# Kernel tuning notes

Hardware: AMD Instinct MI355X
Metric: run time of the kernel (lower is better)

## Reference

```python
import jax, jax.numpy as jnp
import numpy as np

D = 128
H = 4
DK = D // H


def _spmm(row, col, val, x, n):
    # sparse.mm(adj, x) with adj in COO form: out[row] += val * x[col]
    return jax.ops.segment_sum(val[:, None] * x[col], row, num_segments=n)


def _arrg(h, a1_w, a1_b, a2_w, a2_b):
    return jax.nn.leaky_relu(h @ a1_w + a1_b, negative_slope=0.01) @ a2_w + a2_b


def _cross_attn(x, q_x, q_w, k_w, v_w):
    n, d = x.shape
    m = q_x.shape[0]
    q = (q_x @ q_w).reshape(m, H, DK).transpose(1, 0, 2)   # [H, Q, dk]
    k = (x @ k_w).reshape(n, H, DK).transpose(1, 0, 2)     # [H, N, dk]
    v = (q_x @ v_w).reshape(m, H, DK).transpose(1, 0, 2)   # [H, Q, dk]
    s = jnp.einsum('hnd,hqd->hnq', k, q) / jnp.sqrt(jnp.float32(DK))
    w = jax.nn.softmax(s, axis=-1)                          # softmax over queries
    out = jnp.einsum('hnq,hqd->hnd', w, v).transpose(1, 0, 2).reshape(n, d)
    return out + x


def setup_inputs() -> dict:
    key = jax.random.key(0)
    ks = iter(jax.random.split(key, 64))
    nrm = lambda shape, s=0.05: jax.random.normal(next(ks), shape, jnp.float32) * s
    inp = {}
    inp['trans_w'] = nrm((1, D)); inp['trans_b'] = nrm((D,))
    inp['g_w'] = nrm((D, D));     inp['g_b'] = nrm((D,))
    inp['qg_w'] = nrm((D, D));    inp['qg_b'] = nrm((D,))
    inp['q_w'] = nrm((D, D)); inp['k_w'] = nrm((D, D)); inp['v_w'] = nrm((D, D))
    inp['a1_w'] = nrm((D, 2 * D)); inp['a1_b'] = nrm((2 * D,))
    inp['a2_w'] = nrm((2 * D, D)); inp['a2_b'] = nrm((D,))
    inp['x0'] = jax.random.normal(next(ks), (25000,), jnp.float32)
    inp['q0'] = jax.random.normal(next(ks), (100,), jnp.float32)
    for i in (1, 2, 3):
        inp[f'xin{i}'] = jax.random.normal(next(ks), (25000,), jnp.float32)
        inp[f'qin{i}'] = jax.random.normal(next(ks), (100,), jnp.float32)
    n_sizes = {1: 50000, 2: 75000, 3: 100000}
    q_sizes = {1: 200, 2: 300, 3: 400}
    for i in (1, 2, 3):
        e = 16 * n_sizes[i]
        inp[f'aval{i}'] = jax.random.uniform(next(ks), (e,), jnp.float32)
        inp[f'arow{i}'] = jax.random.randint(next(ks), (e,), 0, n_sizes[i], jnp.int64)
        inp[f'acol{i}'] = jax.random.randint(next(ks), (e,), 0, n_sizes[i], jnp.int64)
        qe = 16 * q_sizes[i]
        inp[f'qval{i}'] = jax.random.uniform(next(ks), (qe,), jnp.float32)
        inp[f'qrow{i}'] = jax.random.randint(next(ks), (qe,), 0, q_sizes[i], jnp.int64)
        inp[f'qcol{i}'] = jax.random.randint(next(ks), (qe,), 0, q_sizes[i], jnp.int64)
    return inp


def reference(trans_w, trans_b, g_w, g_b, qg_w, qg_b, q_w, k_w, v_w,
              a1_w, a1_b, a2_w, a2_b,
              x0, q0, xin1, xin2, xin3, qin1, qin2, qin3,
              aval1, aval2, aval3, qval1, qval2, qval3,
              arow1, acol1, arow2, acol2, arow3, acol3,
              qrow1, qcol1, qrow2, qcol2, qrow3, qcol3):
    trans = lambda v: v[:, None] @ trans_w + trans_b
    x = trans(x0)
    qx = trans(q0)
    steps = [
        (xin1, qin1, arow1, acol1, aval1, qrow1, qcol1, qval1, 50000, 200),
        (xin2, qin2, arow2, acol2, aval2, qrow2, qcol2, qval2, 75000, 300),
        (xin3, qin3, arow3, acol3, aval3, qrow3, qcol3, qval3, 100000, 400),
    ]
    for xin, qin, ar, ac, av, qr, qc, qv, n, m in steps:
        x = jnp.concatenate([x, trans(xin)], axis=0)
        qx = jnp.concatenate([qx, trans(qin)], axis=0)
        x = _spmm(ar, ac, av, x @ g_w + g_b, n)
        qx = _spmm(qr, qc, qv, qx @ qg_w + qg_b, m)
        x = _arrg(x, a1_w, a1_b, a2_w, a2_b)
        qx = _arrg(qx, a1_w, a1_b, a2_w, a2_b)
        x = _cross_attn(x, qx, q_w, k_w, v_w)
    return (x, qx)
```

## Files before the change

kernel.cpp:

```cpp
#include <hip/hip_runtime.h>

typedef unsigned short u16;
typedef __attribute__((ext_vector_type(8))) short bf16x8;
typedef __attribute__((ext_vector_type(4))) float f32x4;

__device__ __forceinline__ float b2f(u16 v) {
    return __uint_as_float(((unsigned)v) << 16);
}
__device__ __forceinline__ u16 f2b(float x) {
    unsigned u = __float_as_uint(x);
    unsigned r = u + 0x7FFFu + ((u >> 16) & 1u);
    return (u16)(r >> 16);
}
__device__ __forceinline__ float4 load_bf4(const u16* p) {
    ushort4 q = *(const ushort4*)p;
    float4 f;
    f.x = b2f(q.x); f.y = b2f(q.y); f.z = b2f(q.z); f.w = b2f(q.w);
    return f;
}
__device__ __forceinline__ float4 in4(const void* p, long off, bool bf) {
    if (bf) return load_bf4((const u16*)p + off);
    return *(const float4*)((const float*)p + off);
}
__device__ __forceinline__ float in1(const void* p, long off, bool bf) {
    if (bf) return b2f(((const u16*)p)[off]);
    return ((const float*)p)[off];
}
__device__ __forceinline__ int inIdx(const void* p, long i, bool i64) {
    return ((const int*)p)[i64 ? 2 * i : i];
}

__global__ void sniff_kernel(const u16* __restrict__ x0bits, const int* __restrict__ arow,
                             int* __restrict__ flags) {
    if (threadIdx.x != 0 || blockIdx.x != 0) return;
    int plaus = 0;
    for (int i = 0; i < 256; ++i) {
        u16 v = x0bits[i];
        int e = (v >> 7) & 0xFF;
        if (v == 0 || (e >= 100 && e <= 135)) plaus++;
    }
    flags[0] = (plaus >= 200) ? 1 : 0;
    int nz = 0;
    for (int i = 1; i < 128; i += 2) nz += (arow[i] != 0);
    flags[1] = (nz == 0) ? 1 : 0;
}

__global__ void trans_kernel(const void* __restrict__ v, const void* __restrict__ tw,
                             const void* __restrict__ tb, float* __restrict__ out,
                             int rows, const int* __restrict__ flags) {
    const bool bf = flags[0] != 0;
    int t = blockIdx.x * blockDim.x + threadIdx.x;
    int c4 = (t & 31) * 4;
    int r = t >> 5;
    if (r >= rows) return;
    float vv = in1(v, r, bf);
    float4 w4 = in4(tw, c4, bf);
    float4 b4 = in4(tb, c4, bf);
    float4 o;
    o.x = vv * w4.x + b4.x; o.y = vv * w4.y + b4.y;
    o.z = vv * w4.z + b4.z; o.w = vv * w4.w + b4.w;
    *(float4*)(out + (size_t)r * 128 + c4) = o;
}

__global__ void wprep_kernel(const void* __restrict__ src, u16* __restrict__ dst,
                             int K, int N, const int* __restrict__ flags) {
    const bool bf = flags[0] != 0;
    int idx = blockIdx.x * blockDim.x + threadIdx.x;
    if (idx >= K * N) return;
    int j = idx & 7, lane = (idx >> 3) & 63, t = idx >> 9;
    int KC = K >> 5;
    int kc = t % KC, ct = t / KC;
    int k = kc * 32 + (lane >> 4) * 8 + j;
    int nn = ct * 16 + (lane & 15);
    dst[idx] = f2b(in1(src, (long)k * N + nn, bf));
}

template<int KTOT, int NOUT, bool LEAKY, typename AT, typename CT>
__launch_bounds__(256)
__global__ void gemm_mfma_kernel(const AT* __restrict__ A, const u16* __restrict__ Wf,
                                 const void* __restrict__ bias, CT* __restrict__ C,
                                 int n, const int* __restrict__ flags) {
    constexpr int KC = KTOT / 32;
    constexpr int NT = NOUT / 16;
    __shared__ u16 wlds[KTOT * NOUT];
    {
        const int4* srcw = (const int4*)Wf;
        int4* dstw = (int4*)wlds;
        constexpr int NV = KTOT * NOUT * 2 / 16;
#pragma unroll
        for (int i = 0; i < NV / 256; ++i)
            dstw[i * 256 + threadIdx.x] = srcw[i * 256 + threadIdx.x];
    }
    __syncthreads();
    const bool bf = flags[0] != 0;
    const int lane = threadIdx.x & 63;
    const int wave = threadIdx.x >> 6;
    const int quad = lane >> 4, col = lane & 15;
    const int rbase = (blockIdx.x * 4 + wave) * 16;
    if (rbase >= n) return;
    int node = rbase + col; if (node >= n) node = n - 1;
    f32x4 acc[NT];
#pragma unroll
    for (int ct = 0; ct < NT; ++ct) acc[ct] = (f32x4){0.f, 0.f, 0.f, 0.f};
#pragma unroll
    for (int kc = 0; kc < KC; ++kc) {
        bf16x8 af;
        if constexpr (sizeof(AT) == 2) {
            af = *(const bf16x8*)((const u16*)A + (size_t)node * KTOT + kc * 32 + quad * 8);
        } else {
            const float* ap = (const float*)A + (size_t)node * KTOT + kc * 32 + quad * 8;
            float4 a0 = *(const float4*)ap;
            float4 a1 = *(const float4*)(ap + 4);
            af[0] = (short)f2b(a0.x); af[1] = (short)f2b(a0.y);
            af[2] = (short)f2b(a0.z); af[3] = (short)f2b(a0.w);
            af[4] = (short)f2b(a1.x); af[5] = (short)f2b(a1.y);
            af[6] = (short)f2b(a1.z); af[7] = (short)f2b(a1.w);
        }
#pragma unroll
        for (int ct = 0; ct < NT; ++ct) {
            bf16x8 wf = *(const bf16x8*)(wlds + (((ct * KC + kc) * 64 + lane) * 8));
            acc[ct] = __builtin_amdgcn_mfma_f32_16x16x32_bf16(af, wf, acc[ct], 0, 0, 0);
        }
    }
#pragma unroll
    for (int ct = 0; ct < NT; ++ct) {
        int colg = ct * 16 + col;
        float b = bias ? in1(bias, colg, bf) : 0.f;
#pragma unroll
        for (int r = 0; r < 4; ++r) {
            int row = rbase + quad * 4 + r;
            if (row >= n) continue;
            float v = acc[ct][r] + b;
            if (LEAKY) v = v > 0.f ? v : 0.01f * v;
            if constexpr (sizeof(CT) == 2) C[(size_t)row * NOUT + colg] = (CT)f2b(v);
            else                           C[(size_t)row * NOUT + colg] = (CT)v;
        }
    }
}

#define RSH 8
#define NBC_MAX 512
#define EPB 4096

__global__ void zero_int_kernel(int* __restrict__ p, int n) {
    int i = blockIdx.x * blockDim.x + threadIdx.x;
    if (i < n) p[i] = 0;
}

__global__ void bhist_kernel(const void* __restrict__ rows, int e, int* __restrict__ bcnt,
                             int nbc, const int* __restrict__ flags) {
    __shared__ int hist[NBC_MAX];
    const bool i64 = flags[1] != 0;
    for (int i = threadIdx.x; i < nbc; i += 256) hist[i] = 0;
    __syncthreads();
    int base = blockIdx.x * 8192;
    int end = base + 8192; if (end > e) end = e;
    for (int i = base + threadIdx.x; i < end; i += 256)
        atomicAdd(&hist[inIdx(rows, i, i64) >> RSH], 1);
    __syncthreads();
    for (int i = threadIdx.x; i < nbc; i += 256) {
        int c = hist[i];
        if (c) atomicAdd(&bcnt[i], c);
    }
}

__global__ void scanA_kernel(const int* __restrict__ cnt, int n, int* __restrict__ bsum) {
    int base = blockIdx.x * 2048;
    int s = 0;
    for (int j = threadIdx.x; j < 2048; j += 256) {
        int idx = base + j;
        if (idx < n) s += cnt[idx];
    }
#pragma unroll
    for (int off = 32; off; off >>= 1) s += __shfl_down(s, off);
    __shared__ int ws[4];
    if ((threadIdx.x & 63) == 0) ws[threadIdx.x >> 6] = s;
    __syncthreads();
    if (threadIdx.x == 0) bsum[blockIdx.x] = ws[0] + ws[1] + ws[2] + ws[3];
}
__global__ void scanB_kernel(int* __restrict__ bsum, int nb) {
    if (threadIdx.x == 0) {
        int acc = 0;
        for (int i = 0; i < nb; ++i) { int v = bsum[i]; bsum[i] = acc; acc += v; }
    }
}
__global__ void scanC_kernel(const int* __restrict__ cnt, int n, const int* __restrict__ bsum,
                             int* __restrict__ optr, int* __restrict__ ocur) {
    __shared__ int tsum[256];
    int base = blockIdx.x * 2048 + threadIdx.x * 8;
    int v[8]; int s = 0;
#pragma unroll
    for (int j = 0; j < 8; ++j) {
        int idx = base + j;
        v[j] = (idx < n) ? cnt[idx] : 0;
        s += v[j];
    }
    tsum[threadIdx.x] = s;
    __syncthreads();
    for (int off = 1; off < 256; off <<= 1) {
        int t = (threadIdx.x >= off) ? tsum[threadIdx.x - off] : 0;
        __syncthreads();
        tsum[threadIdx.x] += t;
        __syncthreads();
    }
    int excl = bsum[blockIdx.x] + tsum[threadIdx.x] - s;
#pragma unroll
    for (int j = 0; j < 8; ++j) {
        int idx = base + j;
        if (idx < n) { optr[idx] = excl; ocur[idx] = excl; }
        excl += v[j];
    }
}

__launch_bounds__(256)
__global__ void psort_kernel(const void* __restrict__ rows, const void* __restrict__ colsin,
                             const void* __restrict__ valsin, int e,
                             int* __restrict__ gcur, int2* __restrict__ pack0,
                             int nbc, const int* __restrict__ flags) {
    __shared__ int hist[NBC_MAX];
    __shared__ int scan[NBC_MAX];
    __shared__ int base[NBC_MAX];
    __shared__ int cur[NBC_MAX];
    __shared__ int2 stage[EPB];
    __shared__ u16 binof[EPB];
    const bool bf = flags[0] != 0;
    const bool i64 = flags[1] != 0;
    const int tid = threadIdx.x;
    const long s0 = (long)blockIdx.x * EPB;
    int cnt_e = e - (int)s0; if (cnt_e > EPB) cnt_e = EPB;

    for (int i = tid; i < NBC_MAX; i += 256) hist[i] = 0;
    __syncthreads();
    for (int j = tid; j < cnt_e; j += 256)
        atomicAdd(&hist[inIdx(rows, s0 + j, i64) >> RSH], 1);
    __syncthreads();
    for (int i = tid; i < NBC_MAX; i += 256) scan[i] = hist[i];
    __syncthreads();
    for (int off = 1; off < NBC_MAX; off <<= 1) {
        int a = (tid >= off) ? scan[tid - off] : 0;
        int c = scan[tid + 256 - off];
        __syncthreads();
        scan[tid] += a;
        scan[tid + 256] += c;
        __syncthreads();
    }
    for (int i = tid; i < nbc; i += 256) {
        int h = hist[i];
        cur[i] = scan[i] - h;
        base[i] = h ? atomicAdd(&gcur[i], h) : 0;
    }
    __syncthreads();
    for (int j = tid; j < cnt_e; j += 256) {
        int r = inIdx(rows, s0 + j, i64);
        int bin = r >> RSH;
        int p = atomicAdd(&cur[bin], 1);
        int2 pk;
        pk.x = ((r & ((1 << RSH) - 1)) << 20) | inIdx(colsin, s0 + j, i64);
        pk.y = __float_as_int(in1(valsin, s0 + j, bf));
        stage[p] = pk;
        binof[p] = (u16)bin;
    }
    __syncthreads();
    for (int j = tid; j < cnt_e; j += 256) {
        int bin = binof[j];
        int st = scan[bin] - hist[bin];
        pack0[base[bin] + (j - st)] = stage[j];
    }
}

__launch_bounds__(256)
__global__ void breorder256_kernel(const int2* __restrict__ pack0, const int* __restrict__ bptr,
                                   const int* __restrict__ bend, int2* __restrict__ pack1,
                                   int* __restrict__ rowptr, int* __restrict__ rowend, int n) {
    __shared__ int hist[256], scan[256], cur[256];
    const int b = blockIdx.x;
    const int s = bptr[b], e = bend[b];
    const int tid = threadIdx.x;
    hist[tid] = 0;
    __syncthreads();
    for (int i = s + tid; i < e; i += 256)
        atomicAdd(&hist[(unsigned)pack0[i].x >> 20], 1);
    __syncthreads();
    scan[tid] = hist[tid];
    __syncthreads();
    for (int off = 1; off < 256; off <<= 1) {
        int a = (tid >= off) ? scan[tid - off] : 0;
        __syncthreads();
        scan[tid] += a;
        __syncthreads();
    }
    int st = s + scan[tid] - hist[tid];
    cur[tid] = st;
    int rg = (b << RSH) + tid;
    if (rg < n) { rowptr[rg] = st; rowend[rg] = st + hist[tid]; }
    __syncthreads();
    for (int i = s + tid; i < e; i += 256) {
        int2 pk = pack0[i];
        int rl = (unsigned)pk.x >> 20;
        int p = atomicAdd(&cur[rl], 1);
        pack1[p] = (int2){pk.x & 0xFFFFF, pk.y};
    }
}

__device__ __forceinline__ f32x4 bffma4(float v, uint2 h, f32x4 a) {
    a[0] += v * __uint_as_float(h.x << 16);
    a[1] += v * __uint_as_float(h.x & 0xFFFF0000u);
    a[2] += v * __uint_as_float(h.y << 16);
    a[3] += v * __uint_as_float(h.y & 0xFFFF0000u);
    return a;
}
__global__ void spmm_kernel(const u16* __restrict__ H, const int* __restrict__ rowptr,
                            const int* __restrict__ rowend, const int2* __restrict__ pack,
                            u16* __restrict__ out, int n) {
    int w = threadIdx.x >> 6;
    int lane = threadIdx.x & 63;
    int r = blockIdx.x * 4 + w;
    if (r >= n) return;
    const int half = lane >> 5;
    const int l5 = lane & 31;
    int s = rowptr[r], e = rowend[r];
    f32x4 acc = {0.f, 0.f, 0.f, 0.f};
    int i = s + half;
    for (; i + 6 < e; i += 8) {
        int2 p0 = pack[i], p1 = pack[i + 2], p2 = pack[i + 4], p3 = pack[i + 6];
        uint2 h0 = *(const uint2*)(H + (size_t)p0.x * 128 + l5 * 4);
        uint2 h1 = *(const uint2*)(H + (size_t)p1.x * 128 + l5 * 4);
        uint2 h2 = *(const uint2*)(H + (size_t)p2.x * 128 + l5 * 4);
        uint2 h3 = *(const uint2*)(H + (size_t)p3.x * 128 + l5 * 4);
        acc = bffma4(__int_as_float(p0.y), h0, acc);
        acc = bffma4(__int_as_float(p1.y), h1, acc);
        acc = bffma4(__int_as_float(p2.y), h2, acc);
        acc = bffma4(__int_as_float(p3.y), h3, acc);
    }
    for (; i < e; i += 2) {
        int2 p0 = pack[i];
        uint2 h0 = *(const uint2*)(H + (size_t)p0.x * 128 + l5 * 4);
        acc = bffma4(__int_as_float(p0.y), h0, acc);
    }
    acc[0] += __shfl_xor(acc[0], 32, 64);
    acc[1] += __shfl_xor(acc[1], 32, 64);
    acc[2] += __shfl_xor(acc[2], 32, 64);
    acc[3] += __shfl_xor(acc[3], 32, 64);
    if (half == 0) {
        ushort4 o;
        o.x = f2b(acc[0]); o.y = f2b(acc[1]); o.z = f2b(acc[2]); o.w = f2b(acc[3]);
        *(ushort4*)(out + (size_t)r * 128 + l5 * 4) = o;
    }
}

__global__ void attn_prep_kernel(const float* __restrict__ Qq, const float* __restrict__ Qv,
                                 u16* __restrict__ Qf, u16* __restrict__ Vf,
                                 int m, int mt32) {
    int idx = blockIdx.x * blockDim.x + threadIdx.x;
    int total = 4 * mt32 * 1024;
    if (idx >= total) return;
    const int mt16 = mt32 * 2;
    const float scale = 0.17677669529663687f;
    {
        int j = idx & 7, lane = (idx >> 3) & 63;
        int t = idx >> 9;
        int h = t / mt16, qt = t - h * mt16;
        int dim = ((lane >> 4) & 3) * 8 + j;
        int query = qt * 16 + (lane & 15);
        Qf[idx] = (query < m) ? f2b(Qq[(size_t)query * 128 + h * 32 + dim] * scale) : (u16)0;
    }
    {
        int j = idx & 7, lane = (idx >> 3) & 63;
        int u = idx >> 9;
        int dh = u & 1, t = u >> 1;
        int h = t / mt32, qc = t - h * mt32;
        int query = qc * 32 + ((lane >> 4) & 3) * 8 + j;
        int dim = dh * 16 + (lane & 15);
        Vf[idx] = (query < m) ? f2b(Qv[(size_t)query * 128 + h * 32 + dim]) : (u16)0;
    }
}

__launch_bounds__(256)
__global__ void attn_mfma_kernel(const u16* __restrict__ Kb, const u16* __restrict__ Qf,
                                 const u16* __restrict__ Vf, float* __restrict__ X,
                                 int n, int m, int mt32, int pad) {
    __shared__ u16 Pbuf_all[4 * 16 * 40];
    const int h = blockIdx.y;
    const int wave = threadIdx.x >> 6;
    const int lane = threadIdx.x & 63;
    u16* Pbuf = Pbuf_all + wave * 16 * 40;
    const int nb = (blockIdx.x * 4 + wave) * 16;
    if (nb >= n) return;
    const int quad = lane >> 4, col = lane & 15;
    int node = nb + col; if (node >= n) node = n - 1;
    bf16x8 kf = *(const bf16x8*)(Kb + (size_t)node * 128 + h * 32 + quad * 8);
    f32x4 O0 = {0.f, 0.f, 0.f, 0.f}, O1 = {0.f, 0.f, 0.f, 0.f};
    const f32x4 zero = {0.f, 0.f, 0.f, 0.f};
    float Lp0 = 0.f, Lp1 = 0.f, Lp2 = 0.f, Lp3 = 0.f;
    const u16* Qbase = Qf + (size_t)h * (mt32 * 2) * 512;
    const u16* Vbase = Vf + (size_t)h * mt32 * 1024;
    for (int qc = 0; qc < mt32; ++qc) {
#pragma unroll
        for (int half = 0; half < 2; ++half) {
            bf16x8 qfr = *(const bf16x8*)(Qbase + (size_t)(qc * 2 + half) * 512 + lane * 8);
            f32x4 S = __builtin_amdgcn_mfma_f32_16x16x32_bf16(kf, qfr, zero, 0, 0, 0);
            float e0 = __expf(fminf(S[0], 80.f));
            float e1 = __expf(fminf(S[1], 80.f));
            float e2 = __expf(fminf(S[2], 80.f));
            float e3 = __expf(fminf(S[3], 80.f));
            Lp0 += e0; Lp1 += e1; Lp2 += e2; Lp3 += e3;
            int qoff = half * 16 + col;
            Pbuf[(quad * 4 + 0) * 40 + qoff] = f2b(e0);
            Pbuf[(quad * 4 + 1) * 40 + qoff] = f2b(e1);
            Pbuf[(quad * 4 + 2) * 40 + qoff] = f2b(e2);
            Pbuf[(quad * 4 + 3) * 40 + qoff] = f2b(e3);
        }
        bf16x8 pf = *(const bf16x8*)(Pbuf + col * 40 + quad * 8);
        bf16x8 v0 = *(const bf16x8*)(Vbase + (size_t)(qc * 2 + 0) * 512 + lane * 8);
        bf16x8 v1 = *(const bf16x8*)(Vbase + (size_t)(qc * 2 + 1) * 512 + lane * 8);
        O0 = __builtin_amdgcn_mfma_f32_16x16x32_bf16(pf, v0, O0, 0, 0, 0);
        O1 = __builtin_amdgcn_mfma_f32_16x16x32_bf16(pf, v1, O1, 0, 0, 0);
    }
#pragma unroll
    for (int mask = 1; mask < 16; mask <<= 1) {
        Lp0 += __shfl_xor(Lp0, mask, 64);
        Lp1 += __shfl_xor(Lp1, mask, 64);
        Lp2 += __shfl_xor(Lp2, mask, 64);
        Lp3 += __shfl_xor(Lp3, mask, 64);
    }
    float inv[4];
    inv[0] = 1.f / fmaxf(Lp0 - (float)pad, 1e-35f);
    inv[1] = 1.f / fmaxf(Lp1 - (float)pad, 1e-35f);
    inv[2] = 1.f / fmaxf(Lp2 - (float)pad, 1e-35f);
    inv[3] = 1.f / fmaxf(Lp3 - (float)pad, 1e-35f);
#pragma unroll
    for (int r = 0; r < 4; ++r) {
        int nd = nb + quad * 4 + r;
        if (nd < n) {
            float* xp = X + (size_t)nd * 128 + h * 32;
            xp[col]      += O0[r] * inv[r];
            xp[16 + col] += O1[r] * inv[r];
        }
    }
}

__global__ void out_writer_kernel(const float* __restrict__ in, void* __restrict__ out,
                                  long elem_off, int n4, const int* __restrict__ flags) {
    const bool bf = flags[0] != 0;
    int i = blockIdx.x * blockDim.x + threadIdx.x;
    if (i >= n4) return;
    float4 v = ((const float4*)in)[i];
    if (bf) {
        ushort4 q; q.x = f2b(v.x); q.y = f2b(v.y); q.z = f2b(v.z); q.w = f2b(v.w);
        ((ushort4*)((u16*)out + elem_off))[i] = q;
    } else {
        ((float4*)((float*)out + elem_off))[i] = v;
    }
}

extern "C" void kernel_launch(void* const* d_in, const int* in_sizes, int n_in,
                              void* d_out, int out_size, void* d_ws, size_t ws_size,
                              hipStream_t stream) {
    (void)n_in; (void)out_size; (void)ws_size;
    const void* trans_w = d_in[0];
    const void* trans_b = d_in[1];
    const void* g_w  = d_in[2];
    const void* g_b  = d_in[3];
    const void* qg_w = d_in[4];
    const void* qg_b = d_in[5];
    const void* q_w  = d_in[6];
    const void* k_w  = d_in[7];
    const void* v_w  = d_in[8];
    const void* a1_w = d_in[9];
    const void* a1_b = d_in[10];
    const void* a2_w = d_in[11];
    const void* a2_b = d_in[12];
    const void* x0   = d_in[13];
    const void* q0   = d_in[14];

    int ixin[3], iqin[3], iaval[3], iarow[3], iacol[3], iqval[3], iqrow[3], iqcol[3];
    if (in_sizes[16] == 100) {
        for (int s = 0; s < 3; ++s) {
            ixin[s] = 15 + 2 * s; iqin[s] = 16 + 2 * s;
            int b = 21 + 6 * s;
            iaval[s] = b; iarow[s] = b + 1; iacol[s] = b + 2;
            iqval[s] = b + 3; iqrow[s] = b + 4; iqcol[s] = b + 5;
        }
    } else {
        int xs[3] = {15,16,17}, qs_[3] = {18,19,20};
        int av[3] = {21,22,23}, qv[3] = {24,25,26};
        int ar[3] = {27,29,31}, ac[3] = {28,30,32};
        int qr[3] = {33,35,37}, qc[3] = {34,36,38};
        for (int s = 0; s < 3; ++s) {
            ixin[s]=xs[s]; iqin[s]=qs_[s]; iaval[s]=av[s]; iqval[s]=qv[s];
            iarow[s]=ar[s]; iacol[s]=ac[s]; iqrow[s]=qr[s]; iqcol[s]=qc[s];
        }
    }

    char* p = (char*)d_ws;
    auto alloc = [&](size_t bytes) -> char* {
        char* r = p;
        p += (bytes + 255) & ~(size_t)255;
        return r;
    };
    int*   flags = (int*)alloc(256);
    const int NMAX = 100000;
    float* X   = (float*)alloc((size_t)NMAX * 128 * 4);
    u16*   T1b = (u16*)  alloc((size_t)NMAX * 128 * 2);
    u16*   Xs  = (u16*)  alloc((size_t)NMAX * 128 * 2);
    u16*   T2  = (u16*)  alloc((size_t)NMAX * 256 * 2);
    float* QX  = (float*)alloc((size_t)400 * 128 * 4);
    u16*   QT1b= (u16*)  alloc((size_t)400 * 128 * 2);
    u16*   QXs = (u16*)  alloc((size_t)400 * 128 * 2);
    u16*   QT2 = (u16*)  alloc((size_t)400 * 256 * 2);
    float* Qq  = (float*)alloc((size_t)400 * 128 * 4);
    float* Qv  = (float*)alloc((size_t)400 * 128 * 4);
    u16*   Qfrag = (u16*)alloc((size_t)4 * 13 * 1024 * 2);
    u16*   Vfrag = (u16*)alloc((size_t)4 * 13 * 1024 * 2);
    u16* Wg  = (u16*)alloc((size_t)128 * 128 * 2);
    u16* Wqg = (u16*)alloc((size_t)128 * 128 * 2);
    u16* Wa1 = (u16*)alloc((size_t)128 * 256 * 2);
    u16* Wa2 = (u16*)alloc((size_t)256 * 128 * 2);
    u16* Wk  = (u16*)alloc((size_t)128 * 128 * 2);
    u16* Wq  = (u16*)alloc((size_t)128 * 128 * 2);
    u16* Wv  = (u16*)alloc((size_t)128 * 128 * 2);
    int2*  csr_pack = (int2*)alloc((size_t)1600000 * 8);
    int*   bcnt   = (int*)alloc((size_t)NBC_MAX * 4);
    int*   bktptr = (int*)alloc((size_t)NBC_MAX * 4);
    int*   bktcur = (int*)alloc((size_t)NBC_MAX * 4);
    int*   rowptr = (int*)alloc((size_t)NMAX * 4);
    int*   rowend = (int*)alloc((size_t)NMAX * 4);
    int*   bsum   = (int*)alloc(256);
    int2*  pack0  = (int2*)T2;

    sniff_kernel<<<1, 64, 0, stream>>>((const u16*)x0, (const int*)d_in[iarow[0]], flags);

    auto wprep = [&](const void* src, u16* dst, int K, int N) {
        wprep_kernel<<<(K * N + 255) / 256, 256, 0, stream>>>(src, dst, K, N, flags);
    };
    wprep(g_w,  Wg,  128, 128);
    wprep(qg_w, Wqg, 128, 128);
    wprep(a1_w, Wa1, 128, 256);
    wprep(a2_w, Wa2, 256, 128);
    wprep(k_w,  Wk,  128, 128);
    wprep(q_w,  Wq,  128, 128);
    wprep(v_w,  Wv,  128, 128);

    auto launch_trans = [&](const void* v, float* out, int rows) {
        trans_kernel<<<(rows * 32 + 255) / 256, 256, 0, stream>>>(v, trans_w, trans_b, out, rows, flags);
    };
    auto build_spmm = [&](const void* rows, const void* colsidx, const void* vals, int e,
                          int nrows, const u16* H, u16* OUT) {
        int nbc = (nrows + 255) >> RSH;
        int nsb = (nbc + 2047) / 2048;
        zero_int_kernel<<<(nbc + 255) / 256, 256, 0, stream>>>(bcnt, nbc);
        bhist_kernel<<<(e + 8191) / 8192, 256, 0, stream>>>(rows, e, bcnt, nbc, flags);
        scanA_kernel<<<nsb, 256, 0, stream>>>(bcnt, nbc, bsum);
        scanB_kernel<<<1, 64, 0, stream>>>(bsum, nsb);
        scanC_kernel<<<nsb, 256, 0, stream>>>(bcnt, nbc, bsum, bktptr, bktcur);
        psort_kernel<<<(e + EPB - 1) / EPB, 256, 0, stream>>>(rows, colsidx, vals, e,
                                                              bktcur, pack0, nbc, flags);
        breorder256_kernel<<<nbc, 256, 0, stream>>>(pack0, bktptr, bktcur, csr_pack,
                                                    rowptr, rowend, nrows);
        spmm_kernel<<<(nrows + 3) / 4, 256, 0, stream>>>(H, rowptr, rowend, csr_pack,
                                                         OUT, nrows);
    };

    int nprev = in_sizes[13];
    int mprev = in_sizes[14];
    launch_trans(x0, X, nprev);
    launch_trans(q0, QX, mprev);

    const int ns[3] = {50000, 75000, 100000};
    const int ms[3] = {200, 300, 400};
    for (int s = 0; s < 3; ++s) {
        const int n = ns[s], m = ms[s];
        const int e  = in_sizes[iaval[s]];
        const int qe = in_sizes[iqval[s]];
        launch_trans(d_in[ixin[s]], X + (size_t)nprev * 128, n - nprev);
        launch_trans(d_in[iqin[s]], QX + (size_t)mprev * 128, m - mprev);
        const int gb  = (n + 63) / 64;
        const int gqb = (m + 63) / 64;
        gemm_mfma_kernel<128, 128, false, float, u16><<<gb, 256, 0, stream>>>(X, Wg, g_b, T1b, n, flags);
        build_spmm(d_in[iarow[s]], d_in[iacol[s]], d_in[iaval[s]], e, n, T1b, Xs);
        gemm_mfma_kernel<128, 128, false, float, u16><<<gqb, 256, 0, stream>>>(QX, Wqg, qg_b, QT1b, m, flags);
        build_spmm(d_in[iqrow[s]], d_in[iqcol[s]], d_in[iqval[s]], qe, m, QT1b, QXs);
        gemm_mfma_kernel<128, 256, true, u16, u16><<<gb, 256, 0, stream>>>(Xs, Wa1, a1_b, T2, n, flags);
        gemm_mfma_kernel<256, 128, false, u16, float><<<gb, 256, 0, stream>>>(T2, Wa2, a2_b, X, n, flags);
        gemm_mfma_kernel<128, 256, true, u16, u16><<<gqb, 256, 0, stream>>>(QXs, Wa1, a1_b, QT2, m, flags);
        gemm_mfma_kernel<256, 128, false, u16, float><<<gqb, 256, 0, stream>>>(QT2, Wa2, a2_b, QX, m, flags);
        gemm_mfma_kernel<128, 128, false, float, u16><<<gb, 256, 0, stream>>>(X, Wk, nullptr, T1b, n, flags);
        gemm_mfma_kernel<128, 128, false, float, float><<<gqb, 256, 0, stream>>>(QX, Wq, nullptr, Qq, m, flags);
        gemm_mfma_kernel<128, 128, false, float, float><<<gqb, 256, 0, stream>>>(QX, Wv, nullptr, Qv, m, flags);
        const int mt32 = (m + 31) / 32;
        const int pad = mt32 * 32 - m;
        const int ptot = 4 * mt32 * 1024;
        attn_prep_kernel<<<(ptot + 255) / 256, 256, 0, stream>>>(Qq, Qv, Qfrag, Vfrag, m, mt32);
        attn_mfma_kernel<<<dim3((n + 63) / 64, 4), 256, 0, stream>>>(T1b, Qfrag, Vfrag, X, n, m, mt32, pad);
        nprev = n;
        mprev = m;
    }

    const int n4x = 100000 * 128 / 4;
    const int n4q = 400 * 128 / 4;
    out_writer_kernel<<<(n4x + 255) / 256, 256, 0, stream>>>(X, d_out, 0, n4x, flags);
    out_writer_kernel<<<(n4q + 255) / 256, 256, 0, stream>>>(QX, d_out, (long)100000 * 128, n4q, flags);
}
```

Measured before the change: 1.327 ms.

## Widen attention tiles, use exp2 and transpose-read LDS, fuse Q/V GEMMs and scans

The attention kernel now handles 32 nodes per wave instead of 16, so each Q and V fragment load is shared by two K tiles. It folds log2(e) into the Q scale so it can use the native exp2, packs probabilities with v_cvt_pk_bf16_f32, and reads them back with ds_read_b64_tr_b16 transpose loads. Separately, the Q and V projections are fused into one kernel that shares the A-tile load, and the three-kernel bucket scan is replaced by a single-block scan. This removes several small launches and redundant loads, at the cost of more registers per wave and hand-written inline asm with manual waitcnts.

```diff
diff --git a/kernel.cpp b/kernel.cpp
--- a/kernel.cpp
+++ b/kernel.cpp
@@ -3,6 +3,7 @@
 typedef unsigned short u16;
 typedef __attribute__((ext_vector_type(8))) short bf16x8;
 typedef __attribute__((ext_vector_type(4))) float f32x4;
+typedef __attribute__((ext_vector_type(2))) unsigned u32x2;
 
 __device__ __forceinline__ float b2f(u16 v) {
     return __uint_as_float(((unsigned)v) << 16);
@@ -138,6 +139,67 @@
     }
 }
 
+__launch_bounds__(256)
+__global__ void gemm_qv_kernel(const float* __restrict__ A, const u16* __restrict__ Wfq,
+                               const u16* __restrict__ Wfv, float* __restrict__ Cq,
+                               float* __restrict__ Cv, int n) {
+    __shared__ u16 wldsq[128 * 128];
+    __shared__ u16 wldsv[128 * 128];
+    {
+        const int4* sq = (const int4*)Wfq;
+        const int4* sv = (const int4*)Wfv;
+        int4* dq = (int4*)wldsq;
+        int4* dv = (int4*)wldsv;
+#pragma unroll
+        for (int i = 0; i < 8; ++i) {
+            dq[i * 256 + threadIdx.x] = sq[i * 256 + threadIdx.x];
+            dv[i * 256 + threadIdx.x] = sv[i * 256 + threadIdx.x];
+        }
+    }
+    __syncthreads();
+    const int lane = threadIdx.x & 63;
+    const int wave = threadIdx.x >> 6;
+    const int quad = lane >> 4, col = lane & 15;
+    const int rbase = (blockIdx.x * 4 + wave) * 16;
+    if (rbase >= n) return;
+    int node = rbase + col; if (node >= n) node = n - 1;
+    f32x4 accq[8], accv[8];
+#pragma unroll
+    for (int ct = 0; ct < 8; ++ct) {
+        accq[ct] = (f32x4){0.f, 0.f, 0.f, 0.f};
+        accv[ct] = (f32x4){0.f, 0.f, 0.f, 0.f};
+    }
+#pragma unroll
+    for (int kc = 0; kc < 4; ++kc) {
+        const float* ap = A + (size_t)node * 128 + kc * 32 + quad * 8;
+        float4 a0 = *(const float4*)ap;
+        float4 a1 = *(const float4*)(ap + 4);
+        bf16x8 af;
+        af[0] = (short)f2b(a0.x); af[1] = (short)f2b(a0.y);
+        af[2] = (short)f2b(a0.z); af[3] = (short)f2b(a0.w);
+        af[4] = (short)f2b(a1.x); af[5] = (short)f2b(a1.y);
+        af[6] = (short)f2b(a1.z); af[7] = (short)f2b(a1.w);
+#pragma unroll
+        for (int ct = 0; ct < 8; ++ct) {
+            bf16x8 wq = *(const bf16x8*)(wldsq + (((ct * 4 + kc) * 64 + lane) * 8));
+            bf16x8 wv = *(const bf16x8*)(wldsv + (((ct * 4 + kc) * 64 + lane) * 8));
+            accq[ct] = __builtin_amdgcn_mfma_f32_16x16x32_bf16(af, wq, accq[ct], 0, 0, 0);
+            accv[ct] = __builtin_amdgcn_mfma_f32_16x16x32_bf16(af, wv, accv[ct], 0, 0, 0);
+        }
+    }
+#pragma unroll
+    for (int ct = 0; ct < 8; ++ct) {
+        int colg = ct * 16 + col;
+#pragma unroll
+        for (int r = 0; r < 4; ++r) {
+            int row = rbase + quad * 4 + r;
+            if (row >= n) continue;
+            Cq[(size_t)row * 128 + colg] = accq[ct][r];
+            Cv[(size_t)row * 128 + colg] = accv[ct][r];
+        }
+    }
+}
+
 #define RSH 8
 #define NBC_MAX 512
 #define EPB 4096
@@ -164,52 +226,24 @@
     }
 }
 
-__global__ void scanA_kernel(const int* __restrict__ cnt, int n, int* __restrict__ bsum) {
-    int base = blockIdx.x * 2048;
-    int s = 0;
-    for (int j = threadIdx.x; j < 2048; j += 256) {
-        int idx = base + j;
-        if (idx < n) s += cnt[idx];
-    }
-#pragma unroll
-    for (int off = 32; off; off >>= 1) s += __shfl_down(s, off);
-    __shared__ int ws[4];
-    if ((threadIdx.x & 63) == 0) ws[threadIdx.x >> 6] = s;
-    __syncthreads();
-    if (threadIdx.x == 0) bsum[blockIdx.x] = ws[0] + ws[1] + ws[2] + ws[3];
-}
-__global__ void scanB_kernel(int* __restrict__ bsum, int nb) {
-    if (threadIdx.x == 0) {
-        int acc = 0;
-        for (int i = 0; i < nb; ++i) { int v = bsum[i]; bsum[i] = acc; acc += v; }
-    }
-}
-__global__ void scanC_kernel(const int* __restrict__ cnt, int n, const int* __restrict__ bsum,
+__global__ void scanF_kernel(const int* __restrict__ bcnt, int nbc,
                              int* __restrict__ optr, int* __restrict__ ocur) {
-    __shared__ int tsum[256];
-    int base = blockIdx.x * 2048 + threadIdx.x * 8;
-    int v[8]; int s = 0;
-#pragma unroll
-    for (int j = 0; j < 8; ++j) {
-        int idx = base + j;
-        v[j] = (idx < n) ? cnt[idx] : 0;
-        s += v[j];
-    }
-    tsum[threadIdx.x] = s;
-    __syncthreads();
-    for (int off = 1; off < 256; off <<= 1) {
-        int t = (threadIdx.x >= off) ? tsum[threadIdx.x - off] : 0;
+    __shared__ int sc[NBC_MAX];
+    const int tid = threadIdx.x;
+    int v0 = (tid < nbc) ? bcnt[tid] : 0;
+    int v1 = (tid + 256 < nbc) ? bcnt[tid + 256] : 0;
+    sc[tid] = v0; sc[tid + 256] = v1;
+    __syncthreads();
+    for (int off = 1; off < NBC_MAX; off <<= 1) {
+        int a = (tid >= off) ? sc[tid - off] : 0;
+        int b = sc[tid + 256 - off];
         __syncthreads();
-        tsum[threadIdx.x] += t;
+        sc[tid] += a;
+        sc[tid + 256] += b;
         __syncthreads();
     }
-    int excl = bsum[blockIdx.x] + tsum[threadIdx.x] - s;
-#pragma unroll
-    for (int j = 0; j < 8; ++j) {
-        int idx = base + j;
-        if (idx < n) { optr[idx] = excl; ocur[idx] = excl; }
-        excl += v[j];
-    }
+    if (tid < nbc)       { int x = sc[tid] - v0;       optr[tid] = x;       ocur[tid] = x; }
+    if (tid + 256 < nbc) { int x = sc[tid + 256] - v1; optr[tid + 256] = x; ocur[tid + 256] = x; }
 }
 
 __launch_bounds__(256)
@@ -355,7 +389,7 @@
     int total = 4 * mt32 * 1024;
     if (idx >= total) return;
     const int mt16 = mt32 * 2;
-    const float scale = 0.17677669529663687f;
+    const float scale = 0.17677669529663687f * 1.44269504088896340736f;
     {
         int j = idx & 7, lane = (idx >> 3) & 63;
         int t = idx >> 9;
@@ -379,62 +413,100 @@
 __global__ void attn_mfma_kernel(const u16* __restrict__ Kb, const u16* __restrict__ Qf,
                                  const u16* __restrict__ Vf, float* __restrict__ X,
                                  int n, int m, int mt32, int pad) {
-    __shared__ u16 Pbuf_all[4 * 16 * 40];
+    __shared__ __align__(128) u16 Pbuf_all[4 * 1024];
     const int h = blockIdx.y;
     const int wave = threadIdx.x >> 6;
     const int lane = threadIdx.x & 63;
-    u16* Pbuf = Pbuf_all + wave * 16 * 40;
-    const int nb = (blockIdx.x * 4 + wave) * 16;
+    const int nb = (blockIdx.x * 4 + wave) * 32;
     if (nb >= n) return;
     const int quad = lane >> 4, col = lane & 15;
-    int node = nb + col; if (node >= n) node = n - 1;
-    bf16x8 kf = *(const bf16x8*)(Kb + (size_t)node * 128 + h * 32 + quad * 8);
-    f32x4 O0 = {0.f, 0.f, 0.f, 0.f}, O1 = {0.f, 0.f, 0.f, 0.f};
+    int node0 = nb + col;      if (node0 >= n) node0 = n - 1;
+    int node1 = nb + 16 + col; if (node1 >= n) node1 = n - 1;
+    bf16x8 kf0 = *(const bf16x8*)(Kb + (size_t)node0 * 128 + h * 32 + quad * 8);
+    bf16x8 kf1 = *(const bf16x8*)(Kb + (size_t)node1 * 128 + h * 32 + quad * 8);
+    f32x4 O00 = {0.f, 0.f, 0.f, 0.f}, O01 = {0.f, 0.f, 0.f, 0.f};
+    f32x4 O10 = {0.f, 0.f, 0.f, 0.f}, O11 = {0.f, 0.f, 0.f, 0.f};
     const f32x4 zero = {0.f, 0.f, 0.f, 0.f};
-    float Lp0 = 0.f, Lp1 = 0.f, Lp2 = 0.f, Lp3 = 0.f;
+    float Lp0[4] = {0.f, 0.f, 0.f, 0.f};
+    float Lp1[4] = {0.f, 0.f, 0.f, 0.f};
+    u16* Pw0 = Pbuf_all + wave * 1024;
+    u16* Pw1 = Pw0 + 512;
+    uint2* pw0[2]; uint2* pw1[2];
+    pw0[0] = (uint2*)(Pw0 + col * 16 + quad * 4);
+    pw0[1] = (uint2*)(Pw0 + 256 + col * 16 + quad * 4);
+    pw1[0] = (uint2*)(Pw1 + col * 16 + quad * 4);
+    pw1[1] = (uint2*)(Pw1 + 256 + col * 16 + quad * 4);
+    const unsigned paddr0 = (unsigned)(uintptr_t)Pw0 + (unsigned)(quad * 256 + col * 8);
+    const unsigned paddr1 = (unsigned)(uintptr_t)Pw1 + (unsigned)(quad * 256 + col * 8);
     const u16* Qbase = Qf + (size_t)h * (mt32 * 2) * 512;
     const u16* Vbase = Vf + (size_t)h * mt32 * 1024;
     for (int qc = 0; qc < mt32; ++qc) {
 #pragma unroll
         for (int half = 0; half < 2; ++half) {
             bf16x8 qfr = *(const bf16x8*)(Qbase + (size_t)(qc * 2 + half) * 512 + lane * 8);
-            f32x4 S = __builtin_amdgcn_mfma_f32_16x16x32_bf16(kf, qfr, zero, 0, 0, 0);
-            float e0 = __expf(fminf(S[0], 80.f));
-            float e1 = __expf(fminf(S[1], 80.f));
-            float e2 = __expf(fminf(S[2], 80.f));
-            float e3 = __expf(fminf(S[3], 80.f));
-            Lp0 += e0; Lp1 += e1; Lp2 += e2; Lp3 += e3;
-            int qoff = half * 16 + col;
-            Pbuf[(quad * 4 + 0) * 40 + qoff] = f2b(e0);
-            Pbuf[(quad * 4 + 1) * 40 + qoff] = f2b(e1);
-            Pbuf[(quad * 4 + 2) * 40 + qoff] = f2b(e2);
-            Pbuf[(quad * 4 + 3) * 40 + qoff] = f2b(e3);
-        }
-        bf16x8 pf = *(const bf16x8*)(Pbuf + col * 40 + quad * 8);
+            f32x4 S0 = __builtin_amdgcn_mfma_f32_16x16x32_bf16(kf0, qfr, zero, 0, 0, 0);
+            f32x4 S1 = __builtin_amdgcn_mfma_f32_16x16x32_bf16(kf1, qfr, zero, 0, 0, 0);
+            float a0 = __builtin_amdgcn_exp2f(fminf(S0[0], 115.f));
+            float a1 = __builtin_amdgcn_exp2f(fminf(S0[1], 115.f));
+            float a2 = __builtin_amdgcn_exp2f(fminf(S0[2], 115.f));
+            float a3 = __builtin_amdgcn_exp2f(fminf(S0[3], 115.f));
+            float b0 = __builtin_amdgcn_exp2f(fminf(S1[0], 115.f));
+            float b1 = __builtin_amdgcn_exp2f(fminf(S1[1], 115.f));
+            float b2 = __builtin_amdgcn_exp2f(fminf(S1[2], 115.f));
+            float b3 = __builtin_amdgcn_exp2f(fminf(S1[3], 115.f));
+            Lp0[0] += a0; Lp0[1] += a1; Lp0[2] += a2; Lp0[3] += a3;
+            Lp1[0] += b0; Lp1[1] += b1; Lp1[2] += b2; Lp1[3] += b3;
+            unsigned ra, rb, rc, rd;
+            asm volatile("v_cvt_pk_bf16_f32 %0, %1, %2" : "=v"(ra) : "v"(a0), "v"(a1));
+            asm volatile("v_cvt_pk_bf16_f32 %0, %1, %2" : "=v"(rb) : "v"(a2), "v"(a3));
+            asm volatile("v_cvt_pk_bf16_f32 %0, %1, %2" : "=v"(rc) : "v"(b0), "v"(b1));
+            asm volatile("v_cvt_pk_bf16_f32 %0, %1, %2" : "=v"(rd) : "v"(b2), "v"(b3));
+            uint2 pka; pka.x = ra; pka.y = rb;
+            uint2 pkb; pkb.x = rc; pkb.y = rd;
+            *pw0[half] = pka;
+            *pw1[half] = pkb;
+        }
+        asm volatile("s_waitcnt lgkmcnt(0)" ::: "memory");
+        u32x2 t0a, t0b, t1a, t1b;
+        asm volatile("ds_read_b64_tr_b16 %0, %1" : "=&v"(t0a) : "v"(paddr0) : "memory");
+        asm volatile("ds_read_b64_tr_b16 %0, %1 offset:128" : "=&v"(t0b) : "v"(paddr0) : "memory");
+        asm volatile("ds_read_b64_tr_b16 %0, %1" : "=&v"(t1a) : "v"(paddr1) : "memory");
+        asm volatile("ds_read_b64_tr_b16 %0, %1 offset:128" : "=&v"(t1b) : "v"(paddr1) : "memory");
+        asm volatile("s_waitcnt lgkmcnt(0)" ::: "memory");
+        __builtin_amdgcn_sched_barrier(0);
+        bf16x8 pf0, pf1;
+        ((u32x2*)&pf0)[0] = t0a; ((u32x2*)&pf0)[1] = t0b;
+        ((u32x2*)&pf1)[0] = t1a; ((u32x2*)&pf1)[1] = t1b;
         bf16x8 v0 = *(const bf16x8*)(Vbase + (size_t)(qc * 2 + 0) * 512 + lane * 8);
         bf16x8 v1 = *(const bf16x8*)(Vbase + (size_t)(qc * 2 + 1) * 512 + lane * 8);
-        O0 = __builtin_amdgcn_mfma_f32_16x16x32_bf16(pf, v0, O0, 0, 0, 0);
-        O1 = __builtin_amdgcn_mfma_f32_16x16x32_bf16(pf, v1, O1, 0, 0, 0);
+        O00 = __builtin_amdgcn_mfma_f32_16x16x32_bf16(pf0, v0, O00, 0, 0, 0);
+        O01 = __builtin_amdgcn_mfma_f32_16x16x32_bf16(pf0, v1, O01, 0, 0, 0);
+        O10 = __builtin_amdgcn_mfma_f32_16x16x32_bf16(pf1, v0, O10, 0, 0, 0);
+        O11 = __builtin_amdgcn_mfma_f32_16x16x32_bf16(pf1, v1, O11, 0, 0, 0);
     }
 #pragma unroll
     for (int mask = 1; mask < 16; mask <<= 1) {
-        Lp0 += __shfl_xor(Lp0, mask, 64);
-        Lp1 += __shfl_xor(Lp1, mask, 64);
-        Lp2 += __shfl_xor(Lp2, mask, 64);
-        Lp3 += __shfl_xor(Lp3, mask, 64);
-    }
-    float inv[4];
-    inv[0] = 1.f / fmaxf(Lp0 - (float)pad, 1e-35f);
-    inv[1] = 1.f / fmaxf(Lp1 - (float)pad, 1e-35f);
-    inv[2] = 1.f / fmaxf(Lp2 - (float)pad, 1e-35f);
-    inv[3] = 1.f / fmaxf(Lp3 - (float)pad, 1e-35f);
+#pragma unroll
+        for (int r = 0; r < 4; ++r) {
+            Lp0[r] += __shfl_xor(Lp0[r], mask, 64);
+            Lp1[r] += __shfl_xor(Lp1[r], mask, 64);
+        }
+    }
 #pragma unroll
     for (int r = 0; r < 4; ++r) {
         int nd = nb + quad * 4 + r;
         if (nd < n) {
+            float inv = 1.f / fmaxf(Lp0[r] - (float)pad, 1e-35f);
             float* xp = X + (size_t)nd * 128 + h * 32;
-            xp[col]      += O0[r] * inv[r];
-            xp[16 + col] += O1[r] * inv[r];
+            xp[col]      += O00[r] * inv;
+            xp[16 + col] += O01[r] * inv;
+        }
+        int nd1 = nb + 16 + quad * 4 + r;
+        if (nd1 < n) {
+            float inv = 1.f / fmaxf(Lp1[r] - (float)pad, 1e-35f);
+            float* xp = X + (size_t)nd1 * 128 + h * 32;
+            xp[col]      += O10[r] * inv;
+            xp[16 + col] += O11[r] * inv;
         }
     }
 }
@@ -525,7 +597,6 @@
     int*   bktcur = (int*)alloc((size_t)NBC_MAX * 4);
     int*   rowptr = (int*)alloc((size_t)NMAX * 4);
     int*   rowend = (int*)alloc((size_t)NMAX * 4);
-    int*   bsum   = (int*)alloc(256);
     int2*  pack0  = (int2*)T2;
 
     sniff_kernel<<<1, 64, 0, stream>>>((const u16*)x0, (const int*)d_in[iarow[0]], flags);
@@ -547,12 +618,9 @@
     auto build_spmm = [&](const void* rows, const void* colsidx, const void* vals, int e,
                           int nrows, const u16* H, u16* OUT) {
         int nbc = (nrows + 255) >> RSH;
-        int nsb = (nbc + 2047) / 2048;
         zero_int_kernel<<<(nbc + 255) / 256, 256, 0, stream>>>(bcnt, nbc);
         bhist_kernel<<<(e + 8191) / 8192, 256, 0, stream>>>(rows, e, bcnt, nbc, flags);
-        scanA_kernel<<<nsb, 256, 0, stream>>>(bcnt, nbc, bsum);
-        scanB_kernel<<<1, 64, 0, stream>>>(bsum, nsb);
-        scanC_kernel<<<nsb, 256, 0, stream>>>(bcnt, nbc, bsum, bktptr, bktcur);
+        scanF_kernel<<<1, 256, 0, stream>>>(bcnt, nbc, bktptr, bktcur);
         psort_kernel<<<(e + EPB - 1) / EPB, 256, 0, stream>>>(rows, colsidx, vals, e,
                                                               bktcur, pack0, nbc, flags);
         breorder256_kernel<<<nbc, 256, 0, stream>>>(pack0, bktptr, bktcur, csr_pack,
@@ -585,13 +653,12 @@
         gemm_mfma_kernel<128, 256, true, u16, u16><<<gqb, 256, 0, stream>>>(QXs, Wa1, a1_b, QT2, m, flags);
         gemm_mfma_kernel<256, 128, false, u16, float><<<gqb, 256, 0, stream>>>(QT2, Wa2, a2_b, QX, m, flags);
         gemm_mfma_kernel<128, 128, false, float, u16><<<gb, 256, 0, stream>>>(X, Wk, nullptr, T1b, n, flags);
-        gemm_mfma_kernel<128, 128, false, float, float><<<gqb, 256, 0, stream>>>(QX, Wq, nullptr, Qq, m, flags);
-        gemm_mfma_kernel<128, 128, false, float, float><<<gqb, 256, 0, stream>>>(QX, Wv, nullptr, Qv, m, flags);
+        gemm_qv_kernel<<<gqb, 256, 0, stream>>>(QX, Wq, Wv, Qq, Qv, m);
         const int mt32 = (m + 31) / 32;
         const int pad = mt32 * 32 - m;
         const int ptot = 4 * mt32 * 1024;
         attn_prep_kernel<<<(ptot + 255) / 256, 256, 0, stream>>>(Qq, Qv, Qfrag, Vfrag, m, mt32);
-        attn_mfma_kernel<<<dim3((n + 63) / 64, 4), 256, 0, stream>>>(T1b, Qfrag, Vfrag, X, n, m, mt32, pad);
+        attn_mfma_kernel<<<dim3((n + 127) / 128, 4), 256, 0, stream>>>(T1b, Qfrag, Vfrag, X, n, m, mt32, pad);
         nprev = n;
         mprev = m;
     }
```

Result: faster. 1.282 ms (-3.4%).
